# Performance work log

Measured on AMD Instinct MI355X. Metric: run time of the kernel, lower is better.

## Reference

```python
import jax, jax.numpy as jnp
import numpy as np

N_NODES = 100_000
N_EDGES = 1_600_000
IN_C, OUT_C = 128, 64


def setup_inputs() -> dict:
    key = jax.random.key(0)
    k1, k2, k3, k4 = jax.random.split(key, 4)
    x = jax.random.normal(k1, (N_NODES, IN_C), dtype=jnp.float32)
    # xavier_uniform with relu gain sqrt(2)
    gain = float(np.sqrt(2.0))
    bound = gain * float(np.sqrt(6.0 / (IN_C + OUT_C)))
    weight = jax.random.uniform(k2, (IN_C, OUT_C), minval=-bound, maxval=bound, dtype=jnp.float32)
    bias = jnp.zeros((OUT_C,), dtype=jnp.float32)
    src = jax.random.randint(k3, (N_EDGES,), 0, N_NODES, dtype=jnp.int32)
    dst = jax.random.randint(k4, (N_EDGES,), 0, N_NODES, dtype=jnp.int32)
    return {"x": x, "weight": weight, "bias": bias, "src": src, "dst": dst}


def reference(x, weight, bias, src, dst):
    # DGL GraphConv, norm='both'.
    n = x.shape[0]
    ones = jnp.ones(src.shape, dtype=x.dtype)
    deg_out = jax.ops.segment_sum(ones, src, num_segments=n)  # source out-degree
    deg_in = jax.ops.segment_sum(ones, dst, num_segments=n)   # destination in-degree
    norm_src = jnp.maximum(deg_out, 1.0) ** -0.5
    norm_dst = jnp.maximum(deg_in, 1.0) ** -0.5
    h = x * norm_src[:, None]          # [N, IN]
    # in_channels > out_channels: apply weight before aggregation (DGL fast path)
    h = h @ weight                      # [N, OUT]
    msg = h[src]                        # [E, OUT] gather
    agg = jax.ops.segment_sum(msg, dst, num_segments=n)  # [N, OUT] scatter-add
    return agg * norm_dst[:, None] + bias
```

## Files before the change

### kernel.cpp

```cpp
#include <hip/hip_runtime.h>
#include <hip/hip_bf16.h>

#define N_NODES 100000
#define N_EDGES 1600000
#define IN_C    128
#define OUT_C   64

#define SLOT_W 48
#define CAP    47

#define GEMM_BLK 512
#define FILL_BLK ((N_EDGES + 255) / 256)

typedef __bf16 bf16x8 __attribute__((ext_vector_type(8)));
typedef float  f32x4  __attribute__((ext_vector_type(4)));

#define DEGS_OFF  0
#define CNT_OFF   400000
#define SLOT_OFF  800000
#define H_OFF     20000000

__global__ __launch_bounds__(256) void fused_fill_gemm(
    const float* __restrict__ x, const float* __restrict__ w,
    const int* __restrict__ src, const int* __restrict__ dst,
    int* __restrict__ degs, int* __restrict__ cnt, int* __restrict__ slots,
    __bf16* __restrict__ h) {
  if (blockIdx.x >= GEMM_BLK) {
    const int i = (blockIdx.x - GEMM_BLK) * 256 + threadIdx.x;
    if (i < N_EDGES) {
      const int s = src[i];
      const int d = dst[i];
      atomicAdd(&degs[s], 1);
      const int pos = atomicAdd(&cnt[d], 1);
      if (pos < CAP) slots[d * SLOT_W + pos] = s;
    }
    return;
  }

  const int lane = threadIdx.x & 63;
  const int l15 = lane & 15;
  const int q = lane >> 4;
  const int wave = blockIdx.x * 4 + (threadIdx.x >> 6);
  const int n_waves = GEMM_BLK * 4;
  const int n_groups = N_NODES / 16;

  bf16x8 bfrag[4][4];
#pragma unroll
  for (int kc = 0; kc < 4; ++kc) {
#pragma unroll
    for (int t = 0; t < 4; ++t) {
      bf16x8 tmp;
#pragma unroll
      for (int j = 0; j < 8; ++j)
        tmp[j] = (__bf16)w[(kc * 32 + q * 8 + j) * OUT_C + t * 16 + l15];
      bfrag[kc][t] = tmp;
    }
  }

  for (int g = wave; g < n_groups; g += n_waves) {
    const int n0 = g * 16;
    const float* xp = x + (long)(n0 + l15) * IN_C + q * 8;

    f32x4 acc[4];
#pragma unroll
    for (int t = 0; t < 4; ++t) {
      f32x4 z = {0.f, 0.f, 0.f, 0.f};
      acc[t] = z;
    }

#pragma unroll
    for (int kc = 0; kc < 4; ++kc) {
      f32x4 u = *(const f32x4*)(xp + kc * 32);
      f32x4 v = *(const f32x4*)(xp + kc * 32 + 4);
      bf16x8 a;
#pragma unroll
      for (int j = 0; j < 4; ++j) {
        a[j] = (__bf16)u[j];
        a[4 + j] = (__bf16)v[j];
      }
#pragma unroll
      for (int t = 0; t < 4; ++t)
        acc[t] = __builtin_amdgcn_mfma_f32_16x16x32_bf16(a, bfrag[kc][t], acc[t], 0, 0, 0);
    }

#pragma unroll
    for (int r = 0; r < 4; ++r) {
      const int row = n0 + q * 4 + r;
#pragma unroll
      for (int t = 0; t < 4; ++t)
        h[(long)row * OUT_C + t * 16 + l15] = (__bf16)acc[t][r];
    }
  }
}

__global__ __launch_bounds__(256) void aggregate_kernel(
    const __bf16* __restrict__ h, const int* __restrict__ cnt,
    const int* __restrict__ slots, const int* __restrict__ degs,
    const float* __restrict__ bias, float* __restrict__ out) {
  const int node = blockIdx.x * 4 + (threadIdx.x >> 6);
  if (node >= N_NODES) return;
  const int lane = threadIdx.x & 63;
  const int c = cnt[node];
  const float ndv = rsqrtf((float)(c < 1 ? 1 : c));
  const int end = c < CAP ? c : CAP;
  const int* sl = slots + (long)node * SLOT_W;

  float a0 = 0.f, a1 = 0.f, a2 = 0.f, a3 = 0.f;
  int j = 0;
  for (; j + 4 <= end; j += 4) {
    int s0 = sl[j];
    int s1 = sl[j + 1];
    int s2 = sl[j + 2];
    int s3 = sl[j + 3];
    int d0 = degs[s0], d1 = degs[s1], d2 = degs[s2], d3 = degs[s3];
    float w0 = rsqrtf((float)(d0 < 1 ? 1 : d0));
    float w1 = rsqrtf((float)(d1 < 1 ? 1 : d1));
    float w2 = rsqrtf((float)(d2 < 1 ? 1 : d2));
    float w3 = rsqrtf((float)(d3 < 1 ? 1 : d3));
    a0 += (float)h[(long)s0 * OUT_C + lane] * w0;
    a1 += (float)h[(long)s1 * OUT_C + lane] * w1;
    a2 += (float)h[(long)s2 * OUT_C + lane] * w2;
    a3 += (float)h[(long)s3 * OUT_C + lane] * w3;
  }
  for (; j < end; ++j) {
    int s0 = sl[j];
    int d0 = degs[s0];
    a0 += (float)h[(long)s0 * OUT_C + lane] * rsqrtf((float)(d0 < 1 ? 1 : d0));
  }

  float r = ((a0 + a1) + (a2 + a3)) * ndv + bias[lane];
  out[(long)node * OUT_C + lane] = r;
}

extern "C" void kernel_launch(void* const* d_in, const int* in_sizes, int n_in,
                              void* d_out, int out_size, void* d_ws, size_t ws_size,
                              hipStream_t stream) {
  const float* x    = (const float*)d_in[0];
  const float* w    = (const float*)d_in[1];
  const float* bias = (const float*)d_in[2];
  const int*   src  = (const int*)d_in[3];
  const int*   dst  = (const int*)d_in[4];
  float* out = (float*)d_out;

  char* ws = (char*)d_ws;
  int*    degs  = (int*)(ws + DEGS_OFF);
  int*    cnt   = (int*)(ws + CNT_OFF);
  int*    slots = (int*)(ws + SLOT_OFF);
  __bf16* h     = (__bf16*)(ws + H_OFF);

  hipMemsetAsync(ws, 0, 2 * N_NODES * sizeof(int), stream);

  fused_fill_gemm<<<GEMM_BLK + FILL_BLK, 256, 0, stream>>>(
      x, w, src, dst, degs, cnt, slots, h);

  aggregate_kernel<<<(N_NODES + 3) / 4, 256, 0, stream>>>(
      h, cnt, slots, degs, bias, out);
}
```

Measured before the change: 324.1 us.

## Prescale h by source norm and vectorize aggregation with 16-byte gathers

Adds a separate kernel that multiplies each row of h by the source-degree norm, which removes the per-edge degs lookup and rsqrt from the aggregation loop. The aggregation now processes 8 edges per wave in parallel, with each lane loading 8 bf16 values as one 16-byte load. Partial sums are then reduced across lanes with shuffles and written as vector stores. The costs are an extra kernel launch plus a read-modify-write pass over h, an extra bf16 rounding of the scaled values, and the shuffle reduction.

```diff
diff --git a/kernel.cpp b/kernel.cpp
--- a/kernel.cpp
+++ b/kernel.cpp
@@ -93,43 +93,68 @@
   }
 }
 
+__global__ __launch_bounds__(256) void scale_kernel(
+    __bf16* __restrict__ h, const int* __restrict__ degs) {
+  int tid = blockIdx.x * 256 + threadIdx.x;
+  if (tid >= N_NODES * 8) return;
+  int n = tid >> 3;
+  int c8 = (tid & 7) * 8;
+  int d = degs[n];
+  float s = rsqrtf((float)(d < 1 ? 1 : d));
+  bf16x8* p = (bf16x8*)(h + (long)n * OUT_C + c8);
+  bf16x8 v = *p;
+#pragma unroll
+  for (int k = 0; k < 8; ++k) v[k] = (__bf16)((float)v[k] * s);
+  *p = v;
+}
+
 __global__ __launch_bounds__(256) void aggregate_kernel(
     const __bf16* __restrict__ h, const int* __restrict__ cnt,
-    const int* __restrict__ slots, const int* __restrict__ degs,
-    const float* __restrict__ bias, float* __restrict__ out) {
+    const int* __restrict__ slots, const float* __restrict__ bias,
+    float* __restrict__ out) {
   const int node = blockIdx.x * 4 + (threadIdx.x >> 6);
   if (node >= N_NODES) return;
   const int lane = threadIdx.x & 63;
+  const int eg = lane >> 3;
+  const int c8 = (lane & 7) * 8;
+
   const int c = cnt[node];
   const float ndv = rsqrtf((float)(c < 1 ? 1 : c));
   const int end = c < CAP ? c : CAP;
   const int* sl = slots + (long)node * SLOT_W;
 
-  float a0 = 0.f, a1 = 0.f, a2 = 0.f, a3 = 0.f;
-  int j = 0;
-  for (; j + 4 <= end; j += 4) {
-    int s0 = sl[j];
-    int s1 = sl[j + 1];
-    int s2 = sl[j + 2];
-    int s3 = sl[j + 3];
-    int d0 = degs[s0], d1 = degs[s1], d2 = degs[s2], d3 = degs[s3];
-    float w0 = rsqrtf((float)(d0 < 1 ? 1 : d0));
-    float w1 = rsqrtf((float)(d1 < 1 ? 1 : d1));
-    float w2 = rsqrtf((float)(d2 < 1 ? 1 : d2));
-    float w3 = rsqrtf((float)(d3 < 1 ? 1 : d3));
-    a0 += (float)h[(long)s0 * OUT_C + lane] * w0;
-    a1 += (float)h[(long)s1 * OUT_C + lane] * w1;
-    a2 += (float)h[(long)s2 * OUT_C + lane] * w2;
-    a3 += (float)h[(long)s3 * OUT_C + lane] * w3;
-  }
-  for (; j < end; ++j) {
-    int s0 = sl[j];
-    int d0 = degs[s0];
-    a0 += (float)h[(long)s0 * OUT_C + lane] * rsqrtf((float)(d0 < 1 ? 1 : d0));
+  float acc[8];
+#pragma unroll
+  for (int k = 0; k < 8; ++k) acc[k] = 0.f;
+
+  for (int j = 0; j < end; j += 8) {
+    const int e = j + eg;
+    if (e < end) {
+      const int s = sl[e];
+      bf16x8 v = *(const bf16x8*)(h + (long)s * OUT_C + c8);
+#pragma unroll
+      for (int k = 0; k < 8; ++k) acc[k] += (float)v[k];
+    }
   }
 
-  float r = ((a0 + a1) + (a2 + a3)) * ndv + bias[lane];
-  out[(long)node * OUT_C + lane] = r;
+#pragma unroll
+  for (int mask = 8; mask <= 32; mask <<= 1) {
+#pragma unroll
+    for (int k = 0; k < 8; ++k)
+      acc[k] += __shfl_xor(acc[k], mask, 64);
+  }
+
+  if (lane < 8) {
+    f32x4 r0, r1;
+#pragma unroll
+    for (int k = 0; k < 4; ++k) {
+      r0[k] = acc[k] * ndv + bias[c8 + k];
+      r1[k] = acc[4 + k] * ndv + bias[c8 + 4 + k];
+    }
+    float* op = out + (long)node * OUT_C + c8;
+    *(f32x4*)op = r0;
+    *(f32x4*)(op + 4) = r1;
+  }
 }
 
 extern "C" void kernel_launch(void* const* d_in, const int* in_sizes, int n_in,
@@ -153,6 +178,8 @@
   fused_fill_gemm<<<GEMM_BLK + FILL_BLK, 256, 0, stream>>>(
       x, w, src, dst, degs, cnt, slots, h);
 
+  scale_kernel<<<(N_NODES * 8 + 255) / 256, 256, 0, stream>>>(h, degs);
+
   aggregate_kernel<<<(N_NODES + 3) / 4, 256, 0, stream>>>(
-      h, cnt, slots, degs, bias, out);
+      h, cnt, slots, bias, out);
 }
```

Result: faster. 302.8 us (-6.6%).
